# Optimization experiments

Measured on AMD Instinct MI355X. Metric: run time of the kernel, lower is better.

Reference implementation:

```python
import jax, jax.numpy as jnp
import numpy as np

HEADS, DIM_HEAD, LANDMARKS, PINV_ITERS, RES_K = 8, 64, 256, 6, 33
DIM = 512


def layer_norm(x, w, b, eps=1e-5):
    mu = x.mean(-1, keepdims=True)
    var = ((x - mu) ** 2).mean(-1, keepdims=True)
    return (x - mu) * jax.lax.rsqrt(var + eps) * w + b


def moore_penrose_pinv(x, iters=PINV_ITERS):
    # x: (b, h, m, m)
    abs_x = jnp.abs(x)
    col = abs_x.sum(-1)
    row = abs_x.sum(-2)
    z = jnp.swapaxes(x, -1, -2) / (jnp.max(col) * jnp.max(row))
    I = jnp.eye(x.shape[-1], dtype=x.dtype)
    for _ in range(iters):
        xz = x @ z
        z = 0.25 * z @ (13.0 * I - xz @ (15.0 * I - xz @ (7.0 * I - xz)))
    return z


def nystrom_attention(x, qkv_w, out_w, out_b, res_kernel):
    b, n, _ = x.shape
    h, dh, m = HEADS, DIM_HEAD, LANDMARKS
    l = n // m  # seq chosen divisible by landmarks
    qkv = x @ qkv_w  # (b, n, 3*h*dh)
    q, k, v = jnp.split(qkv, 3, axis=-1)
    def to_heads(t):
        return t.reshape(b, n, h, dh).transpose(0, 2, 1, 3)  # (b,h,n,dh)
    q, k, v = to_heads(q), to_heads(k), to_heads(v)
    q = q * (dh ** -0.5)
    # landmark pooling: mean over contiguous groups of size l
    q_l = q.reshape(b, h, m, l, dh).mean(axis=3)  # (b,h,m,dh)
    k_l = k.reshape(b, h, m, l, dh).mean(axis=3)
    attn1 = jax.nn.softmax(jnp.einsum('bhid,bhjd->bhij', q, k_l), axis=-1)   # (b,h,n,m)
    attn2 = jax.nn.softmax(jnp.einsum('bhid,bhjd->bhij', q_l, k_l), axis=-1) # (b,h,m,m)
    attn3 = jax.nn.softmax(jnp.einsum('bhid,bhjd->bhij', q_l, k), axis=-1)   # (b,h,m,n)
    attn2_inv = moore_penrose_pinv(attn2)
    out = (attn1 @ attn2_inv) @ (attn3 @ v)  # (b,h,n,dh)
    # depthwise residual conv over sequence dim, per head
    pad = (RES_K - 1) // 2
    out = out + jax.lax.conv_general_dilated(
        v, res_kernel, window_strides=(1, 1), padding=((pad, pad), (0, 0)),
        dimension_numbers=('NCHW', 'OIHW', 'NCHW'), feature_group_count=h)
    out = out.transpose(0, 2, 1, 3).reshape(b, n, h * dh)
    return out @ out_w + out_b


def trans_layer(x, p):
    return x + nystrom_attention(layer_norm(x, p['norm_w'], p['norm_b']),
                                 p['qkv_w'], p['out_w'], p['out_b'], p['res_k'])


def setup_inputs() -> dict:
    key = jax.random.key(0)
    ks = jax.random.split(key, 20)
    N, F = 16383, 1024
    d = {}
    d['x'] = jax.random.normal(ks[0], (1, N, F), dtype=jnp.float32)
    d['fc_w'] = jax.random.normal(ks[1], (F, DIM), dtype=jnp.float32) * 0.03
    d['fc_b'] = jnp.zeros((DIM,), dtype=jnp.float32)
    d['cls_token'] = jax.random.normal(ks[2], (1, 1, DIM), dtype=jnp.float32) * 1e-6
    for i, base in [(3, 'l1'), (9, 'l2')]:
        d[base + '_norm_w'] = jnp.ones((DIM,), dtype=jnp.float32)
        d[base + '_norm_b'] = jnp.zeros((DIM,), dtype=jnp.float32)
        d[base + '_qkv_w'] = jax.random.normal(ks[i], (DIM, 3 * DIM), dtype=jnp.float32) * 0.03
        d[base + '_out_w'] = jax.random.normal(ks[i + 1], (DIM, DIM), dtype=jnp.float32) * 0.03
        d[base + '_out_b'] = jnp.zeros((DIM,), dtype=jnp.float32)
        d[base + '_res_k'] = jax.random.normal(ks[i + 2], (HEADS, 1, RES_K, 1), dtype=jnp.float32) * 0.1
    d['norm_w'] = jnp.ones((DIM,), dtype=jnp.float32)
    d['norm_b'] = jnp.zeros((DIM,), dtype=jnp.float32)
    d['clf_w'] = jax.random.normal(ks[15], (DIM, 4), dtype=jnp.float32) * 0.05
    d['clf_b'] = jnp.zeros((4,), dtype=jnp.float32)
    return d


def reference(x, fc_w, fc_b, cls_token, l1_norm_w, l1_norm_b, l1_qkv_w, l1_out_w,
              l1_out_b, l1_res_k, l2_norm_w, l2_norm_b, l2_qkv_w, l2_out_w,
              l2_out_b, l2_res_k, norm_w, norm_b, clf_w, clf_b):
    h = jax.nn.relu(x @ fc_w + fc_b)                       # (1, N, 512)
    h = jnp.concatenate([cls_token, h], axis=1)            # (1, N+1, 512)
    p1 = dict(norm_w=l1_norm_w, norm_b=l1_norm_b, qkv_w=l1_qkv_w,
              out_w=l1_out_w, out_b=l1_out_b, res_k=l1_res_k)
    p2 = dict(norm_w=l2_norm_w, norm_b=l2_norm_b, qkv_w=l2_qkv_w,
              out_w=l2_out_w, out_b=l2_out_b, res_k=l2_res_k)
    h = trans_layer(h, p1)
    h = trans_layer(h, p2)
    h = layer_norm(h, norm_w, norm_b)[:, 0]                # (1, 512)
    logits = h @ clf_w + clf_b                             # (1, n_classes)
    hazards = jax.nn.sigmoid(logits)
    S = jnp.cumprod(1.0 - hazards, axis=1)
    return (hazards, S)
```

## Files before the change

### kernel.cpp

```cpp
#include <hip/hip_runtime.h>

#define NTOK 16384
#define NDIM 512
#define STP_LD 280

typedef __attribute__((ext_vector_type(8))) short short8;
typedef __attribute__((ext_vector_type(4))) float f32x4;

__device__ __forceinline__ unsigned short f2bf(float f) {
  unsigned u = __float_as_uint(f);
  u += 0x7fffu + ((u >> 16) & 1u);
  return (unsigned short)(u >> 16);
}
__device__ __forceinline__ float bf2f(unsigned short u) {
  return __uint_as_float((unsigned)u << 16);
}

__device__ __forceinline__ void gload_lds16(const void* g, void* l) {
  __builtin_amdgcn_global_load_lds(
      (const __attribute__((address_space(1))) unsigned int*)(unsigned long long)(g),
      (__attribute__((address_space(3))) unsigned int*)(unsigned long long)(l), 16, 0, 0);
}

template<int EPI>
__global__ __launch_bounds__(256) void gemm_bf16(
    const unsigned short* __restrict__ A, const unsigned short* __restrict__ Bt,
    float* __restrict__ C, const float* __restrict__ bias,
    int M, int N, int K, int Mstore)
{
  __shared__ unsigned short As[2][128 * 32];
  __shared__ unsigned short Bs[2][128 * 32];
  const int tid = threadIdx.x;
  const int row0 = blockIdx.y * 128, col0 = blockIdx.x * 128;
  const int wave = tid >> 6, lane = tid & 63;
  const int wm = (wave >> 1) * 64, wn = (wave & 1) * 64;
  const int quad = lane >> 4, m16 = lane & 15;

  const int r0 = tid >> 2;
  const int c8 = (tid & 3) * 8;
  const unsigned short* Ag0 = A + (size_t)(row0 + r0) * K + c8;
  const unsigned short* Ag1 = A + (size_t)(row0 + r0 + 64) * K + c8;
  const unsigned short* Bg0 = Bt + (size_t)(col0 + r0) * K + c8;
  const unsigned short* Bg1 = Bt + (size_t)(col0 + r0 + 64) * K + c8;
  char* AsB = (char*)As;
  char* BsB = (char*)Bs;
  const int wb = wave * 1024;

  f32x4 acc[4][4] = {};
  const int nc = K >> 5;
  gload_lds16(Ag0, AsB + wb);
  gload_lds16(Ag1, AsB + 4096 + wb);
  gload_lds16(Bg0, BsB + wb);
  gload_lds16(Bg1, BsB + 4096 + wb);
  __syncthreads();
  int b = 0;
  for (int c = 0; c < nc; c++) {
    if (c + 1 < nc) {
      int k1 = (c + 1) * 32;
      gload_lds16(Ag0 + k1, AsB + (b ^ 1) * 8192 + wb);
      gload_lds16(Ag1 + k1, AsB + (b ^ 1) * 8192 + 4096 + wb);
      gload_lds16(Bg0 + k1, BsB + (b ^ 1) * 8192 + wb);
      gload_lds16(Bg1 + k1, BsB + (b ^ 1) * 8192 + 4096 + wb);
    }
    short8 af[4], bf[4];
#pragma unroll
    for (int i = 0; i < 4; i++) {
      af[i] = *(const short8*)&As[b][(wm + i * 16 + m16) * 32 + quad * 8];
      bf[i] = *(const short8*)&Bs[b][(wn + i * 16 + m16) * 32 + quad * 8];
    }
#pragma unroll
    for (int i = 0; i < 4; i++)
#pragma unroll
      for (int j = 0; j < 4; j++)
        acc[i][j] = __builtin_amdgcn_mfma_f32_16x16x32_bf16(af[i], bf[j], acc[i][j], 0, 0, 0);
    __syncthreads();
    b ^= 1;
  }
#pragma unroll
  for (int i = 0; i < 4; i++) {
#pragma unroll
    for (int r = 0; r < 4; r++) {
      int gr = row0 + wm + i * 16 + quad * 4 + r;
      if (gr < Mstore) {
#pragma unroll
        for (int j = 0; j < 4; j++) {
          int gc = col0 + wn + j * 16 + m16;
          float v = acc[i][j][r];
          if (EPI == 1) { v += bias[gc]; v = fmaxf(v, 0.f); }
          if (EPI == 2) { v += bias[gc] + C[(size_t)gr * N + gc]; }
          C[(size_t)gr * N + gc] = v;
        }
      }
    }
  }
}

template<bool WN, bool WT, bool WF>
__global__ __launch_bounds__(256) void bmm_pinv64(
    const unsigned short* __restrict__ A, const unsigned short* __restrict__ Bt,
    unsigned short* __restrict__ Cn, unsigned short* __restrict__ Ct,
    float* __restrict__ Cf,
    float an, float bn, float at, float bt)
{
  const int hh = blockIdx.z;
  A  += (size_t)hh << 16;
  Bt += (size_t)hh << 16;
  __shared__ unsigned short As[2][64 * 32];
  __shared__ unsigned short Bs[2][64 * 32];
  const int tid = threadIdx.x;
  const int row0 = blockIdx.y * 64, col0 = blockIdx.x * 64;
  const int wave = tid >> 6, lane = tid & 63;
  const int wm = (wave >> 1) * 32, wn = (wave & 1) * 32;
  const int quad = lane >> 4, m16 = lane & 15;
  const int sr = wave * 16 + (lane >> 2);
  const int sc = (lane & 3) * 8;
  const unsigned short* Ag = A + (size_t)(row0 + sr) * 256 + sc;
  const unsigned short* Bg = Bt + (size_t)(col0 + sr) * 256 + sc;
  char* AsW = (char*)As + wave * 1024;
  char* BsW = (char*)Bs + wave * 1024;

  f32x4 acc[2][2] = {};
  gload_lds16(Ag, AsW);
  gload_lds16(Bg, BsW);
  __syncthreads();
  int b = 0;
  for (int c = 0; c < 8; c++) {
    if (c < 7) {
      gload_lds16(Ag + (c + 1) * 32, AsW + (b ^ 1) * 4096);
      gload_lds16(Bg + (c + 1) * 32, BsW + (b ^ 1) * 4096);
    }
    short8 af[2], bfr[2];
#pragma unroll
    for (int i = 0; i < 2; i++) {
      af[i]  = *(const short8*)&As[b][(wm + i * 16 + m16) * 32 + quad * 8];
      bfr[i] = *(const short8*)&Bs[b][(wn + i * 16 + m16) * 32 + quad * 8];
    }
#pragma unroll
    for (int i = 0; i < 2; i++)
#pragma unroll
      for (int j = 0; j < 2; j++)
        acc[i][j] = __builtin_amdgcn_mfma_f32_16x16x32_bf16(af[i], bfr[j], acc[i][j], 0, 0, 0);
    __syncthreads();
    b ^= 1;
  }
  unsigned short* CnH = Cn + ((size_t)hh << 16);
  unsigned short* CtH = Ct + ((size_t)hh << 16);
  float* CfH = WF ? (Cf + ((size_t)hh << 16)) : nullptr;
#pragma unroll
  for (int i = 0; i < 2; i++) {
#pragma unroll
    for (int r = 0; r < 4; r++) {
      int gr = row0 + wm + i * 16 + quad * 4 + r;
#pragma unroll
      for (int j = 0; j < 2; j++) {
        int gc = col0 + wn + j * 16 + m16;
        float p = acc[i][j][r];
        float diag = (gr == gc) ? 1.f : 0.f;
        if (WN) {
          unsigned short nb_ = f2bf(an * p + bn * diag);
          CnH[(size_t)gr * 256 + gc] = nb_;
          if (WF) CfH[(size_t)gr * 256 + gc] = bf2f(nb_);
        }
        if (WT) CtH[(size_t)gc * 256 + gr] = f2bf(at * p + bt * diag);
      }
    }
  }
}

__global__ void castpad_x(const float* __restrict__ x, unsigned short* __restrict__ xb,
                          size_t nvalid) {
  size_t i4 = ((size_t)blockIdx.x * 256 + threadIdx.x) * 4;
  float4 v = make_float4(0.f, 0.f, 0.f, 0.f);
  if (i4 < nvalid) v = *(const float4*)(x + i4);
  ushort4 o;
  o.x = f2bf(v.x); o.y = f2bf(v.y); o.z = f2bf(v.z); o.w = f2bf(v.w);
  *(ushort4*)(xb + i4) = o;
}

__global__ __launch_bounds__(256) void transpose_cast(
    const float* __restrict__ in, unsigned short* __restrict__ out, int R, int C)
{
  __shared__ float tile[32][33];
  int r0 = blockIdx.x * 32, c0 = blockIdx.y * 32;
  int tx = threadIdx.x & 31, ty = threadIdx.x >> 5;
  for (int yy = ty; yy < 32; yy += 8)
    tile[yy][tx] = in[(size_t)(r0 + yy) * C + c0 + tx];
  __syncthreads();
  for (int yy = ty; yy < 32; yy += 8)
    out[(size_t)(c0 + yy) * R + r0 + tx] = f2bf(tile[tx][yy]);
}

__global__ __launch_bounds__(1024) void qkv_prep(
    const float* __restrict__ qkv,
    unsigned short* __restrict__ qb, unsigned short* __restrict__ kb,
    float* __restrict__ q_l, float* __restrict__ k_lT,
    unsigned short* __restrict__ q_lb, unsigned short* __restrict__ k_lb)
{
  const int j = blockIdx.x, t = threadIdx.x;
  const int cs = t & 255, rg = t >> 8;
  const int c = cs * 4;
  const bool isq = c < 512;
  __shared__ float4 pbuf[4][256];
  float4 acc = make_float4(0.f, 0.f, 0.f, 0.f);
  for (int r = rg * 16; r < rg * 16 + 16; r++) {
    int row = j * 64 + r;
    float4 v = *(const float4*)(qkv + (size_t)row * 1536 + c);
    acc.x += v.x; acc.y += v.y; acc.z += v.z; acc.w += v.w;
    ushort4 o;
    if (isq) {
      o.x = f2bf(v.x * 0.125f); o.y = f2bf(v.y * 0.125f);
      o.z = f2bf(v.z * 0.125f); o.w = f2bf(v.w * 0.125f);
      *(ushort4*)(qb + (size_t)row * 512 + c) = o;
    } else {
      o.x = f2bf(v.x); o.y = f2bf(v.y); o.z = f2bf(v.z); o.w = f2bf(v.w);
      *(ushort4*)(kb + (size_t)row * 512 + (c - 512)) = o;
    }
  }
  pbuf[rg][cs] = acc;
  __syncthreads();
  if (rg == 0) {
    float4 a0 = pbuf[0][cs], a1 = pbuf[1][cs], a2 = pbuf[2][cs], a3 = pbuf[3][cs];
    float sc = (1.f / 64.f) * (isq ? 0.125f : 1.f);
    float4 p;
    p.x = (a0.x + a1.x + a2.x + a3.x) * sc;
    p.y = (a0.y + a1.y + a2.y + a3.y) * sc;
    p.z = (a0.z + a1.z + a2.z + a3.z) * sc;
    p.w = (a0.w + a1.w + a2.w + a3.w) * sc;
    int cc = isq ? c : c - 512;
    int hh = cc >> 6, d = cc & 63;
    size_t o = ((size_t)(hh * 256 + j)) * 64 + d;
    ushort4 ob;
    ob.x = f2bf(p.x); ob.y = f2bf(p.y); ob.z = f2bf(p.z); ob.w = f2bf(p.w);
    if (isq) {
      *(float4*)(q_l + o) = p; *(ushort4*)(q_lb + o) = ob;
    } else {
      size_t of = ((size_t)hh << 14) + (j >> 6) * 4096 + (d >> 5) * 2048
                + ((j >> 4) & 3) * 512 + ((d >> 3) & 3) * 128 + (j & 15) * 8 + (d & 7);
      *(ushort4*)(k_lb + of) = ob;
      float* kt = k_lT + ((size_t)hh * 64 + d) * 256 + j;
      kt[0] = p.x; kt[256] = p.y; kt[512] = p.z; kt[768] = p.w;
    }
  }
}

__global__ __launch_bounds__(256) void transpose_cast_v(
    const float* __restrict__ qkv, unsigned short* __restrict__ vTb)
{
  __shared__ float tile[32][33];
  int i0 = blockIdx.x * 32, c0 = blockIdx.y * 32;
  int tx = threadIdx.x & 31, ty = threadIdx.x >> 5;
  for (int yy = ty; yy < 32; yy += 8)
    tile[yy][tx] = qkv[(size_t)(i0 + yy) * 1536 + 1024 + c0 + tx];
  __syncthreads();
  for (int yy = ty; yy < 32; yy += 8)
    vTb[(size_t)(c0 + yy) * NTOK + i0 + tx] = f2bf(tile[tx][yy]);
}

__global__ __launch_bounds__(256) void conv_seq(
    const unsigned short* __restrict__ vTb, const float* __restrict__ res_k,
    unsigned short* __restrict__ convT)
{
  const int c = blockIdx.y;
  const int h = c >> 6;
  const int i0 = (blockIdx.x * 256 + threadIdx.x) * 8;
  float rk[33];
#pragma unroll
  for (int u = 0; u < 33; u++) rk[u] = res_k[h * 33 + u];
  const unsigned short* vr = vTb + (size_t)c * NTOK;
  float win[40];
#pragma unroll
  for (int ch = 0; ch < 5; ch++) {
    int a = i0 - 16 + ch * 8;
    if (a >= 0 && a < NTOK) {
      ushort4 u0 = *(const ushort4*)(vr + a);
      ushort4 u1 = *(const ushort4*)(vr + a + 4);
      win[ch * 8 + 0] = bf2f(u0.x); win[ch * 8 + 1] = bf2f(u0.y);
      win[ch * 8 + 2] = bf2f(u0.z); win[ch * 8 + 3] = bf2f(u0.w);
      win[ch * 8 + 4] = bf2f(u1.x); win[ch * 8 + 5] = bf2f(u1.y);
      win[ch * 8 + 6] = bf2f(u1.z); win[ch * 8 + 7] = bf2f(u1.w);
    } else {
#pragma unroll
      for (int u = 0; u < 8; u++) win[ch * 8 + u] = 0.f;
    }
  }
  ushort4 o0, o1;
  float out[8];
#pragma unroll
  for (int jj = 0; jj < 8; jj++) {
    float s = 0.f;
#pragma unroll
    for (int u = 0; u < 33; u++) s += rk[u] * win[jj + u];
    out[jj] = s;
  }
  o0.x = f2bf(out[0]); o0.y = f2bf(out[1]); o0.z = f2bf(out[2]); o0.w = f2bf(out[3]);
  o1.x = f2bf(out[4]); o1.y = f2bf(out[5]); o1.z = f2bf(out[6]); o1.w = f2bf(out[7]);
  *(ushort4*)(convT + (size_t)c * NTOK + i0) = o0;
  *(ushort4*)(convT + (size_t)c * NTOK + i0 + 4) = o1;
}

template<bool W2>
__global__ __launch_bounds__(256) void bmm_f32(
    const float* __restrict__ A, const float* __restrict__ B, float* __restrict__ C,
    float* __restrict__ C2, int M, int N, int K, float alpha, float beta, float gamma)
{
  const int h = blockIdx.z;
  A += (size_t)h * M * K; B += (size_t)h * K * N;
  size_t cb = (size_t)h * M * N;
  __shared__ float As[16][64];
  __shared__ float Bs[16][64];
  const int tid = threadIdx.x;
  const int row0 = blockIdx.y * 64, col0 = blockIdx.x * 64;
  const int ty = tid >> 4, tx = tid & 15;
  const int ar = tid >> 2, ac = (tid & 3) << 2;
  const int bk = tid >> 4, bj = (tid & 15) << 2;
  float acc[4][4] = {};
  float4 a  = *(const float4*)(A + (size_t)(row0 + ar) * K + ac);
  float4 bv = *(const float4*)(B + (size_t)bk * N + col0 + bj);
  for (int k0 = 0; k0 < K; k0 += 16) {
    As[ac + 0][ar] = a.x; As[ac + 1][ar] = a.y; As[ac + 2][ar] = a.z; As[ac + 3][ar] = a.w;
    *(float4*)&Bs[bk][bj] = bv;
    __syncthreads();
    if (k0 + 16 < K) {
      a  = *(const float4*)(A + (size_t)(row0 + ar) * K + k0 + 16 + ac);
      bv = *(const float4*)(B + (size_t)(k0 + 16 + bk) * N + col0 + bj);
    }
#pragma unroll
    for (int kk = 0; kk < 16; kk++) {
      float4 av = *(float4*)&As[kk][ty << 2];
      float4 bvv = *(float4*)&Bs[kk][tx << 2];
      float a4[4] = {av.x, av.y, av.z, av.w};
      float b4[4] = {bvv.x, bvv.y, bvv.z, bvv.w};
#pragma unroll
      for (int ii = 0; ii < 4; ii++)
#pragma unroll
        for (int jj = 0; jj < 4; jj++) acc[ii][jj] += a4[ii] * b4[jj];
    }
    __syncthreads();
  }
#pragma unroll
  for (int ii = 0; ii < 4; ii++) {
    int gr = row0 + (ty << 2) + ii;
#pragma unroll
    for (int jj = 0; jj < 4; jj++) {
      int gc = col0 + (tx << 2) + jj;
      float diag = (gr == gc) ? 1.f : 0.f;
      float v = alpha * acc[ii][jj] + beta * diag;
      C[cb + (size_t)gr * N + gc] = v;
      if (W2) C2[cb + (size_t)gr * N + gc] = gamma * diag - v;
    }
  }
}

__global__ void cls_copy(const float* __restrict__ cls, float* __restrict__ h) {
  int t = threadIdx.x;
  if (t < 512) h[t] = cls[t];
}

__global__ __launch_bounds__(256) void layernorm_rows(
    const float* __restrict__ x, unsigned short* __restrict__ y,
    const float* __restrict__ w, const float* __restrict__ b)
{
  const int row = blockIdx.x, tid = threadIdx.x;
  const float* xr = x + (size_t)row * NDIM;
  float2 v = ((const float2*)xr)[tid];
  float sum = v.x + v.y, sq = v.x * v.x + v.y * v.y;
#pragma unroll
  for (int off = 32; off; off >>= 1) { sum += __shfl_xor(sum, off); sq += __shfl_xor(sq, off); }
  __shared__ float r1[4], r2[4];
  if ((tid & 63) == 0) { r1[tid >> 6] = sum; r2[tid >> 6] = sq; }
  __syncthreads();
  sum = r1[0] + r1[1] + r1[2] + r1[3];
  sq  = r2[0] + r2[1] + r2[2] + r2[3];
  float mu = sum * (1.f / 512.f);
  float var = sq * (1.f / 512.f) - mu * mu;
  float rs = rsqrtf(var + 1e-5f);
  float a = (v.x - mu) * rs * w[2 * tid]     + b[2 * tid];
  float c = (v.y - mu) * rs * w[2 * tid + 1] + b[2 * tid + 1];
  ((unsigned*)(y + (size_t)row * NDIM))[tid] = (unsigned)f2bf(a) | ((unsigned)f2bf(c) << 16);
}

__global__ __launch_bounds__(256) void attn2_softmax(
    const float* __restrict__ q_l, const float* __restrict__ k_lT,
    float* __restrict__ x2, unsigned short* __restrict__ x2b)
{
  int row = blockIdx.x, h = blockIdx.y, j = threadIdx.x;
  __shared__ float qrow[64];
  __shared__ float red[4];
  if (j < 64) qrow[j] = q_l[(size_t)(h * 256 + row) * 64 + j];
  __syncthreads();
  const float* kt = k_lT + ((size_t)h * 64) * 256 + j;
  float s = 0.f;
#pragma unroll 8
  for (int d = 0; d < 64; d++) s += qrow[d] * kt[(size_t)d * 256];
  float m = s;
#pragma unroll
  for (int off = 32; off; off >>= 1) m = fmaxf(m, __shfl_xor(m, off));
  if ((j & 63) == 0) red[j >> 6] = m;
  __syncthreads();
  m = fmaxf(fmaxf(red[0], red[1]), fmaxf(red[2], red[3]));
  __syncthreads();
  float e = __expf(s - m), l = e;
#pragma unroll
  for (int off = 32; off; off >>= 1) l += __shfl_xor(l, off);
  if ((j & 63) == 0) red[j >> 6] = l;
  __syncthreads();
  l = red[0] + red[1] + red[2] + red[3];
  float val = e / l;
  size_t o = ((size_t)(h * 256 + row) << 8) + j;
  x2[o] = val;
  x2b[o] = f2bf(val);
}

__global__ __launch_bounds__(256) void colrow_max(const float* __restrict__ x2,
                                                  float* __restrict__ scal)
{
  const int h = blockIdx.x, tid = threadIdx.x;
  const float* xh = x2 + ((size_t)h << 16);
  float mx = -1e30f;
  if (blockIdx.y == 0) {
    const int wave = tid >> 6, lane = tid & 63;
    for (int r = wave; r < 256; r += 4) {
      float4 v = *(const float4*)(xh + (size_t)r * 256 + lane * 4);
      float s = v.x + v.y + v.z + v.w;
#pragma unroll
      for (int off = 32; off; off >>= 1) s += __shfl_xor(s, off);
      mx = fmaxf(mx, s);
    }
  } else {
    float cs = 0.f;
    for (int r0 = 0; r0 < 256; r0 += 8) {
      float v[8];
#pragma unroll
      for (int u = 0; u < 8; u++) v[u] = xh[(size_t)(r0 + u) * 256 + tid];
#pragma unroll
      for (int u = 0; u < 8; u++) cs += v[u];
    }
    mx = cs;
  }
#pragma unroll
  for (int off = 32; off; off >>= 1) mx = fmaxf(mx, __shfl_xor(mx, off));
  __shared__ float red[4];
  if ((tid & 63) == 0) red[tid >> 6] = mx;
  __syncthreads();
  if (tid == 0) {
    float m = fmaxf(fmaxf(red[0], red[1]), fmaxf(red[2], red[3]));
    atomicMax((unsigned int*)&scal[blockIdx.y], __float_as_uint(m));
  }
}

__global__ void zinit_bf(const float* __restrict__ x2, unsigned short* __restrict__ zb,
                         unsigned short* __restrict__ zTb, const float* __restrict__ scal)
{
  int idx = blockIdx.x * 256 + threadIdx.x;
  int hh = idx >> 16, i = (idx >> 8) & 255, j = idx & 255;
  float den = scal[0] * scal[1];
  float val = x2[idx] / den;
  unsigned short b = f2bf(val);
  zTb[idx] = b;
  zb[(hh << 16) + (j << 8) + i] = b;
}

__global__ __launch_bounds__(256) void flash_fused(
    const unsigned short* __restrict__ q_lb, const unsigned short* __restrict__ kb,
    const unsigned short* __restrict__ vTb,
    float* __restrict__ Opart, float* __restrict__ mlpart)
{
  const int ks = blockIdx.x, qg = blockIdx.y, h = blockIdx.z;
  const int tid = threadIdx.x;
  const int wave = tid >> 6, lane = tid & 63;
  const int quad = lane >> 4, m16 = lane & 15;

  __shared__ unsigned short Ks[2][4096];
  __shared__ unsigned short Vs[2][4096];
  __shared__ unsigned short pbuf_all[4][16 * 72];
  unsigned short* pbuf = pbuf_all[wave];

  const int key00 = ks * 512;

  const int sr  = (wave << 3) + (lane >> 3);
  const int sxz = (lane & 7) ^ ((lane >> 3) & 7);
  const unsigned short* kst0 = kb + (size_t)(key00 + sr) * 512 + (h << 6) + sxz * 8;
  const unsigned short* kst1 = kst0 + (size_t)32 * 512;
  const unsigned short* vst0 = vTb + (size_t)((h << 6) + sr) * NTOK + key00 + sxz * 8;
  const unsigned short* vst1 = vst0 + (size_t)32 * NTOK;
  char* ldsKw = (char*)&Ks[0][0] + (wave << 10);
  char* ldsVw = (char*)&Vs[0][0] + (wave << 10);

  const int xs  = m16 & 7;
  const int co0 = ((quad) ^ xs) << 3;
  const int co1 = ((4 + quad) ^ xs) << 3;

  const int qrow_w = qg * 64 + wave * 16;
  const unsigned short* qbase = q_lb + ((size_t)h << 14) + (size_t)(qrow_w + m16) * 64;
  short8 aq0 = *(const short8*)(qbase + quad * 8);
  short8 aq1 = *(const short8*)(qbase + 32 + quad * 8);

  float m_e[4], l_e[4];
#pragma unroll
  for (int e = 0; e < 4; e++) { m_e[e] = -1e30f; l_e[e] = 0.f; }
  f32x4 acc_o[4] = {};

#define FF_STAGE(bb, cc) do {                                   \
    size_t ko = (size_t)(cc) * 32768; int vo = (cc) * 64;       \
    gload_lds16(kst0 + ko, ldsKw + (bb) * 8192);                \
    gload_lds16(kst1 + ko, ldsKw + (bb) * 8192 + 4096);         \
    gload_lds16(vst0 + vo, ldsVw + (bb) * 8192);                \
    gload_lds16(vst1 + vo, ldsVw + (bb) * 8192 + 4096);         \
  } while (0)

  FF_STAGE(0, 0);
  __syncthreads();
  int b = 0;
  for (int c = 0; c < 8; c++) {
    if (c < 7) FF_STAGE(b ^ 1, c + 1);
    const unsigned short* Kb = Ks[b];
    const unsigned short* Vb = Vs[b];
    f32x4 s[4] = {};
    __builtin_amdgcn_s_setprio(1);
#pragma unroll
    for (int kt = 0; kt < 4; kt++) {
      const unsigned short* krow = Kb + ((kt << 4) + m16) * 64;
      short8 b0 = *(const short8*)(krow + co0);
      short8 b1 = *(const short8*)(krow + co1);
      s[kt] = __builtin_amdgcn_mfma_f32_16x16x32_bf16(aq0, b0, s[kt], 0, 0, 0);
      s[kt] = __builtin_amdgcn_mfma_f32_16x16x32_bf16(aq1, b1, s[kt], 0, 0, 0);
    }
    __builtin_amdgcn_s_setprio(0);
#pragma unroll
    for (int e = 0; e < 4; e++) {
      float mx = fmaxf(fmaxf(s[0][e], s[1][e]), fmaxf(s[2][e], s[3][e]));
      mx = fmaxf(mx, __shfl_xor(mx, 1));
      mx = fmaxf(mx, __shfl_xor(mx, 2));
      mx = fmaxf(mx, __shfl_xor(mx, 4));
      mx = fmaxf(mx, __shfl_xor(mx, 8));
      float mn = fmaxf(m_e[e], mx);
      float scale = __expf(m_e[e] - mn);
      m_e[e] = mn;
      float sum = 0.f;
#pragma unroll
      for (int kt = 0; kt < 4; kt++) {
        float ev = __expf(s[kt][e] - mn);
        s[kt][e] = ev;
        sum += ev;
      }
      sum += __shfl_xor(sum, 1); sum += __shfl_xor(sum, 2);
      sum += __shfl_xor(sum, 4); sum += __shfl_xor(sum, 8);
      l_e[e] = l_e[e] * scale + sum;
#pragma unroll
      for (int dt = 0; dt < 4; dt++) acc_o[dt][e] *= scale;
    }
#pragma unroll
    for (int kt = 0; kt < 4; kt++)
#pragma unroll
      for (int e = 0; e < 4; e++)
        pbuf[(quad * 4 + e) * 72 + kt * 16 + m16] = f2bf(s[kt][e]);
    asm volatile("s_waitcnt lgkmcnt(0)" ::: "memory");
    short8 ap0 = *(const short8*)&pbuf[m16 * 72 + quad * 8];
    short8 ap1 = *(const short8*)&pbuf[m16 * 72 + 32 + quad * 8];
    __builtin_amdgcn_s_setprio(1);
#pragma unroll
    for (int dt = 0; dt < 4; dt++) {
      const unsigned short* vrow = Vb + ((dt << 4) + m16) * 64;
      short8 bv0 = *(const short8*)(vrow + co0);
      short8 bv1 = *(const short8*)(vrow + co1);
      acc_o[dt] = __builtin_amdgcn_mfma_f32_16x16x32_bf16(ap0, bv0, acc_o[dt], 0, 0, 0);
      acc_o[dt] = __builtin_amdgcn_mfma_f32_16x16x32_bf16(ap1, bv1, acc_o[dt], 0, 0, 0);
    }
    __builtin_amdgcn_s_setprio(0);
    __syncthreads();
    b ^= 1;
  }
#undef FF_STAGE
  float* ob = Opart + ((size_t)(ks * 8 + h) * 256 + qrow_w) * 64;
#pragma unroll
  for (int dt = 0; dt < 4; dt++)
#pragma unroll
    for (int e = 0; e < 4; e++)
      ob[(size_t)(quad * 4 + e) * 64 + dt * 16 + m16] = acc_o[dt][e];
  if (m16 == 0) {
    float* mlb = mlpart + ((size_t)(ks * 8 + h) * 256 + qrow_w) * 2;
#pragma unroll
    for (int e = 0; e < 4; e++) {
      mlb[(quad * 4 + e) * 2]     = m_e[e];
      mlb[(quad * 4 + e) * 2 + 1] = l_e[e];
    }
  }
}

__global__ __launch_bounds__(256) void flash_merge(
    const float* __restrict__ Opart, const float* __restrict__ mlpart,
    float* __restrict__ kv)
{
  const int rc = blockIdx.x, h = blockIdx.y, tid = threadIdx.x;
  const int r = rc * 32 + (tid >> 3);
  const int d0 = (tid & 7) * 8;
  float M = -1e30f;
  for (int ks = 0; ks < 32; ks++)
    M = fmaxf(M, mlpart[((size_t)(ks * 8 + h) * 256 + r) * 2]);
  float L = 0.f;
  float o[8];
#pragma unroll
  for (int j = 0; j < 8; j++) o[j] = 0.f;
  for (int ks = 0; ks < 32; ks++) {
    const float* mlb = mlpart + ((size_t)(ks * 8 + h) * 256 + r) * 2;
    float w = __expf(mlb[0] - M);
    L += mlb[1] * w;
    const float* op = Opart + ((size_t)(ks * 8 + h) * 256 + r) * 64 + d0;
    float4 a = *(const float4*)op;
    float4 b = *(const float4*)(op + 4);
    o[0] += a.x * w; o[1] += a.y * w; o[2] += a.z * w; o[3] += a.w * w;
    o[4] += b.x * w; o[5] += b.y * w; o[6] += b.z * w; o[7] += b.w * w;
  }
  float invL = 1.f / L;
  float* out = kv + ((size_t)(h * 256 + r)) * 64 + d0;
#pragma unroll
  for (int j = 0; j < 8; j++) out[j] = o[j] * invL;
}

__global__ __launch_bounds__(256) void bmt_kernel(
    const float* __restrict__ zf, const float* __restrict__ kv,
    unsigned short* __restrict__ BmT)
{
  const int jb = blockIdx.x, hh = blockIdx.y, tid = threadIdx.x;
  __shared__ float zt[64 * 256];
  const float* zsrc = zf + ((size_t)hh << 16) + (size_t)(jb * 64) * 256;
  for (int rep = 0; rep < 16; rep++) {
    int e4 = (rep * 256 + tid) * 4;
    *(float4*)&zt[e4] = *(const float4*)(zsrc + e4);
  }
  __syncthreads();
  const int d = tid & 63, jg = tid >> 6;
  const float* kvh = kv + ((size_t)hh << 14) + d;
  float acc[16];
#pragma unroll
  for (int u = 0; u < 16; u++) acc[u] = 0.f;
  for (int k0 = 0; k0 < 256; k0 += 8) {
    float kv8[8];
#pragma unroll
    for (int u = 0; u < 8; u++) kv8[u] = kvh[(size_t)(k0 + u) << 6];
#pragma unroll
    for (int jj = 0; jj < 16; jj++) {
      const float* zr = &zt[(jg * 16 + jj) * 256 + k0];
#pragma unroll
      for (int u = 0; u < 8; u++) acc[jj] += zr[u] * kv8[u];
    }
  }
  unsigned short* obh = BmT + ((size_t)hh << 14) + (d >> 5) * 8192
                        + ((d >> 4) & 1) * 512 + (d & 15) * 8;
#pragma unroll
  for (int jj = 0; jj < 16; jj++) {
    int j = jb * 64 + jg * 16 + jj;
    obh[(j >> 5) * 1024 + ((j >> 3) & 3) * 128 + (j & 7)] = f2bf(acc[jj]);
  }
}

__global__ __launch_bounds__(256) void attn1_out(
    const unsigned short* __restrict__ qb, const unsigned short* __restrict__ k_lb,
    const unsigned short* __restrict__ BmT, const unsigned short* __restrict__ convT,
    unsigned short* __restrict__ attn_out)
{
  const int qc = blockIdx.x, h = blockIdx.y, tid = threadIdx.x;
  const int q0 = qc * 32;
  const int wave = tid >> 6, lane = tid & 63;
  const int quad = lane >> 4, m16 = lane & 15;

  __shared__ unsigned short stp[32 * STP_LD];
  __shared__ float redm[4][32], redl[4][32];

  const int mi3 = (wave & 1) * 16;
  const int nbase = (wave >> 1) * 32;
  const int gi0 = q0 + mi3 + quad * 4;
  ushort4 cv4_[2];
#pragma unroll
  for (int t = 0; t < 2; t++) {
    int d = nbase + t * 16 + m16;
    cv4_[t] = *(const ushort4*)(convT + (size_t)((h << 6) + d) * NTOK + gi0);
  }

  f32x4 acc1[2][4] = {};
  {
    const unsigned short* qbase = qb + (size_t)q0 * 512 + (h << 6);
    const unsigned short* kf = k_lb + ((size_t)h << 14) + (wave << 12);
#pragma unroll
    for (int kc = 0; kc < 2; kc++) {
      short8 aq[2], bk[4];
#pragma unroll
      for (int i = 0; i < 2; i++)
        aq[i] = *(const short8*)(qbase + (size_t)(i * 16 + m16) * 512 + kc * 32 + quad * 8);
#pragma unroll
      for (int n = 0; n < 4; n++)
        bk[n] = *(const short8*)(kf + kc * 2048 + n * 512 + lane * 8);
#pragma unroll
      for (int i = 0; i < 2; i++)
#pragma unroll
        for (int n = 0; n < 4; n++)
          acc1[i][n] = __builtin_amdgcn_mfma_f32_16x16x32_bf16(aq[i], bk[n], acc1[i][n], 0, 0, 0);
    }
  }
#pragma unroll
  for (int i = 0; i < 2; i++) {
#pragma unroll
    for (int e = 0; e < 4; e++) {
      float mx = fmaxf(fmaxf(acc1[i][0][e], acc1[i][1][e]), fmaxf(acc1[i][2][e], acc1[i][3][e]));
      mx = fmaxf(mx, __shfl_xor(mx, 1));
      mx = fmaxf(mx, __shfl_xor(mx, 2));
      mx = fmaxf(mx, __shfl_xor(mx, 4));
      mx = fmaxf(mx, __shfl_xor(mx, 8));
      if (m16 == 0) redm[wave][i * 16 + quad * 4 + e] = mx;
    }
  }
  __syncthreads();
#pragma unroll
  for (int i = 0; i < 2; i++) {
#pragma unroll
    for (int e = 0; e < 4; e++) {
      int r = i * 16 + quad * 4 + e;
      float gm = fmaxf(fmaxf(redm[0][r], redm[1][r]), fmaxf(redm[2][r], redm[3][r]));
      float s = 0.f;
#pragma unroll
      for (int n = 0; n < 4; n++) {
        float ev = __expf(acc1[i][n][e] - gm);
        acc1[i][n][e] = ev;
        s += ev;
      }
      s += __shfl_xor(s, 1); s += __shfl_xor(s, 2);
      s += __shfl_xor(s, 4); s += __shfl_xor(s, 8);
      if (m16 == 0) redl[wave][r] = s;
    }
  }
#pragma unroll
  for (int i = 0; i < 2; i++)
#pragma unroll
    for (int n = 0; n < 4; n++) {
      int col = wave * 64 + n * 16 + m16;
#pragma unroll
      for (int e = 0; e < 4; e++)
        stp[(i * 16 + quad * 4 + e) * STP_LD + col] = f2bf(acc1[i][n][e]);
    }
  __syncthreads();

  f32x4 acc3[2] = {};
  {
    const unsigned short* bf_ = BmT + ((size_t)h << 14) + ((nbase >> 5) << 13);
#pragma unroll
    for (int kc = 0; kc < 8; kc++) {
      short8 ap = *(const short8*)&stp[(mi3 + m16) * STP_LD + kc * 32 + quad * 8];
#pragma unroll
      for (int t = 0; t < 2; t++) {
        short8 bp = *(const short8*)(bf_ + kc * 1024 + t * 512 + lane * 8);
        acc3[t] = __builtin_amdgcn_mfma_f32_16x16x32_bf16(ap, bp, acc3[t], 0, 0, 0);
      }
    }
  }
#pragma unroll
  for (int t = 0; t < 2; t++) {
    int d = nbase + t * 16 + m16;
    unsigned short cvs[4] = {cv4_[t].x, cv4_[t].y, cv4_[t].z, cv4_[t].w};
#pragma unroll
    for (int e = 0; e < 4; e++) {
      int lr = mi3 + quad * 4 + e;
      float l = redl[0][lr] + redl[1][lr] + redl[2][lr] + redl[3][lr];
      float v = acc3[t][e] / l + bf2f(cvs[e]);
      attn_out[((size_t)(gi0 + e) << 9) + (h << 6) + d] = f2bf(v);
    }
  }
}

__global__ __launch_bounds__(256) void final_head(
    const float* __restrict__ hrow, const float* __restrict__ nw, const float* __restrict__ nb,
    const float* __restrict__ cw, const float* __restrict__ cb, float* __restrict__ out)
{
  const int tid = threadIdx.x;
  __shared__ float ln0[512];
  __shared__ float r1[4], r2[4];
  __shared__ float lg[4][4];
  float2 v = ((const float2*)hrow)[tid];
  float sum = v.x + v.y, sq = v.x * v.x + v.y * v.y;
#pragma unroll
  for (int off = 32; off; off >>= 1) { sum += __shfl_xor(sum, off); sq += __shfl_xor(sq, off); }
  if ((tid & 63) == 0) { r1[tid >> 6] = sum; r2[tid >> 6] = sq; }
  __syncthreads();
  sum = r1[0] + r1[1] + r1[2] + r1[3];
  sq  = r2[0] + r2[1] + r2[2] + r2[3];
  float mu = sum * (1.f / 512.f);
  float var = sq * (1.f / 512.f) - mu * mu;
  float rs = rsqrtf(var + 1e-5f);
  ln0[2 * tid]     = (v.x - mu) * rs * nw[2 * tid]     + nb[2 * tid];
  ln0[2 * tid + 1] = (v.y - mu) * rs * nw[2 * tid + 1] + nb[2 * tid + 1];
  __syncthreads();
  float p[4] = {0.f, 0.f, 0.f, 0.f};
  for (int k = tid; k < 512; k += 256) {
    float lv = ln0[k];
#pragma unroll
    for (int c = 0; c < 4; c++) p[c] += lv * cw[k * 4 + c];
  }
#pragma unroll
  for (int off = 32; off; off >>= 1)
#pragma unroll
    for (int c = 0; c < 4; c++) p[c] += __shfl_xor(p[c], off);
  if ((tid & 63) == 0) {
    int w = tid >> 6;
#pragma unroll
    for (int c = 0; c < 4; c++) lg[w][c] = p[c];
  }
  __syncthreads();
  if (tid == 0) {
    float cum = 1.f;
    for (int c = 0; c < 4; c++) {
      float logit = lg[0][c] + lg[1][c] + lg[2][c] + lg[3][c] + cb[c];
      float hz = 1.f / (1.f + __expf(-logit));
      out[c] = hz;
      cum *= (1.f - hz);
      out[4 + c] = cum;
    }
  }
}

extern "C" void kernel_launch(void* const* d_in, const int* in_sizes, int n_in,
                              void* d_out, int out_size, void* d_ws, size_t ws_size,
                              hipStream_t stream)
{
  (void)in_sizes; (void)n_in; (void)out_size; (void)ws_size;
  const float* x    = (const float*)d_in[0];
  const float* fc_w = (const float*)d_in[1];
  const float* fc_b = (const float*)d_in[2];
  const float* cls  = (const float*)d_in[3];
  const float* nw[2]   = {(const float*)d_in[4],  (const float*)d_in[10]};
  const float* nb[2]   = {(const float*)d_in[5],  (const float*)d_in[11]};
  const float* qkvw[2] = {(const float*)d_in[6],  (const float*)d_in[12]};
  const float* outw[2] = {(const float*)d_in[7],  (const float*)d_in[13]};
  const float* outb[2] = {(const float*)d_in[8],  (const float*)d_in[14]};
  const float* resk[2] = {(const float*)d_in[9],  (const float*)d_in[15]};
  const float* fnw = (const float*)d_in[16];
  const float* fnb = (const float*)d_in[17];
  const float* cw  = (const float*)d_in[18];
  const float* cb  = (const float*)d_in[19];

  float* ws = (float*)d_ws;
  float* h    = ws; ws += (size_t)NTOK * NDIM;
  float* qkv  = ws; ws += (size_t)NTOK * 1536;
  float* bigv = ws; ws += (size_t)(512 * NTOK) / 2;
  float* q_l  = ws; ws += 8 * 256 * 64;
  float* k_lT = ws; ws += 8 * 256 * 64;
  float* x2   = ws; ws += 8 * 256 * 256;
  float* zf   = ws; ws += 8 * 256 * 256;
  float* zfin = ws; ws += 8 * 256 * 256;
  float* tA   = ws; ws += 8 * 256 * 256;
  float* tB   = ws; ws += 8 * 256 * 256;
  float* tC   = ws; ws += 8 * 256 * 256;
  float* kv   = ws; ws += 8 * 256 * 64;
  float* scal = ws; ws += 64;
  unsigned short* actb = (unsigned short*)ws; ws += (size_t)NTOK * NDIM / 2;
  unsigned short* wT   = (unsigned short*)ws; ws += (1536 * 512) / 2;
  unsigned short* qb   = (unsigned short*)ws; ws += (size_t)NTOK * NDIM / 2;
  unsigned short* k_lb = (unsigned short*)ws; ws += (8 * 256 * 64) / 2;
  unsigned short* q_lb = (unsigned short*)ws; ws += (8 * 256 * 64) / 2;
  unsigned short* x2b  = (unsigned short*)ws; ws += (8 * 256 * 256) / 2;
  unsigned short* zb0  = (unsigned short*)ws; ws += (8 * 256 * 256) / 2;
  unsigned short* zb1  = (unsigned short*)ws; ws += (8 * 256 * 256) / 2;
  unsigned short* zT0  = (unsigned short*)ws; ws += (8 * 256 * 256) / 2;
  unsigned short* zT1  = (unsigned short*)ws; ws += (8 * 256 * 256) / 2;
  unsigned short* xzb  = (unsigned short*)ws; ws += (8 * 256 * 256) / 2;
  unsigned short* t1T  = (unsigned short*)ws; ws += (8 * 256 * 256) / 2;
  unsigned short* t2T  = (unsigned short*)ws; ws += (8 * 256 * 256) / 2;
  unsigned short* t3T  = (unsigned short*)ws; ws += (8 * 256 * 256) / 2;
  unsigned short* BmT  = (unsigned short*)ws; ws += (8 * 64 * 256) / 2;

  unsigned short* xb  = (unsigned short*)qkv;
  unsigned short* kb  = actb;
  unsigned short* vTb = (unsigned short*)bigv;
  float* Opart  = qkv;
  float* mlpart = qkv + (size_t)32 * 8 * 256 * 64;
  unsigned short* convT = (unsigned short*)(qkv + (size_t)32 * 8 * 256 * 64 + 32 * 8 * 256 * 2);

  unsigned short* zbp[2] = {zb0, zb1};
  unsigned short* zTp[2] = {zT0, zT1};

  castpad_x<<<16384, 256, 0, stream>>>(x, xb, (size_t)16383 * 1024);
  transpose_cast<<<dim3(32, 16), 256, 0, stream>>>(fc_w, wT, 1024, 512);
  gemm_bf16<1><<<dim3(4, 128), 256, 0, stream>>>(xb, wT, h + 512, fc_b,
                                                 16384, 512, 1024, 16383);
  cls_copy<<<1, 512, 0, stream>>>(cls, h);

  for (int L = 0; L < 2; L++) {
    layernorm_rows<<<NTOK, 256, 0, stream>>>(h, actb, nw[L], nb[L]);
    transpose_cast<<<dim3(16, 48), 256, 0, stream>>>(qkvw[L], wT, 512, 1536);
    gemm_bf16<0><<<dim3(12, 128), 256, 0, stream>>>(actb, wT, qkv, nullptr,
                                                    NTOK, 1536, 512, NTOK);
    qkv_prep<<<256, 1024, 0, stream>>>(qkv, qb, kb, q_l, k_lT, q_lb, k_lb);
    transpose_cast_v<<<dim3(512, 16), 256, 0, stream>>>(qkv, vTb);
    attn2_softmax<<<dim3(256, 8), 256, 0, stream>>>(q_l, k_lT, x2, x2b);
    hipMemsetAsync(scal, 0, 2 * sizeof(float), stream);
    colrow_max<<<dim3(8, 2), 256, 0, stream>>>(x2, scal);
    zinit_bf<<<2048, 256, 0, stream>>>(x2, zbp[0], zTp[0], scal);

    flash_fused<<<dim3(32, 4, 8), 256, 0, stream>>>(q_lb, kb, vTb, Opart, mlpart);
    flash_merge<<<dim3(8, 8), 256, 0, stream>>>(Opart, mlpart, kv);
    conv_seq<<<dim3(8, 512), 256, 0, stream>>>(vTb, resk[L], convT);

    int cur = 0;
    dim3 pg(4, 4, 8);
    for (int it = 0; it < 5; it++) {
      bmm_pinv64<true,  true, false><<<pg, 256, 0, stream>>>(x2b, zTp[cur], xzb, t1T, nullptr,
                                                             1.f, 0.f, -1.f, 7.f);
      bmm_pinv64<false, true, false><<<pg, 256, 0, stream>>>(xzb, t1T, nullptr, t2T, nullptr,
                                                             0.f, 0.f, -1.f, 15.f);
      bmm_pinv64<false, true, false><<<pg, 256, 0, stream>>>(xzb, t2T, nullptr, t3T, nullptr,
                                                             0.f, 0.f, -1.f, 13.f);
      if (it < 4)
        bmm_pinv64<true, true, false><<<pg, 256, 0, stream>>>(zbp[cur], t3T, zbp[cur ^ 1],
                                                              zTp[cur ^ 1], nullptr,
                                                              0.25f, 0.f, 0.25f, 0.f);
      else
        bmm_pinv64<true, true, true><<<pg, 256, 0, stream>>>(zbp[cur], t3T, zbp[cur ^ 1],
                                                             zTp[cur ^ 1], zf,
                                                             0.25f, 0.f, 0.25f, 0.f);
      cur ^= 1;
    }
    bmm_f32<true ><<<dim3(4, 4, 8), 256, 0, stream>>>(x2, zf, tA, tB, 256, 256, 256, 1.f, 0.f, 7.f);
    bmm_f32<false><<<dim3(4, 4, 8), 256, 0, stream>>>(tA, tB, tC, nullptr, 256, 256, 256, -1.f, 15.f, 0.f);
    bmm_f32<false><<<dim3(4, 4, 8), 256, 0, stream>>>(tA, tC, tB, nullptr, 256, 256, 256, -1.f, 13.f, 0.f);
    bmm_f32<false><<<dim3(4, 4, 8), 256, 0, stream>>>(zf, tB, zfin, nullptr, 256, 256, 256, 0.25f, 0.f, 0.f);

    bmt_kernel<<<dim3(4, 8), 256, 0, stream>>>(zfin, kv, BmT);
    attn1_out<<<dim3(512, 8), 256, 0, stream>>>(qb, k_lb, BmT, convT, actb);
    transpose_cast<<<dim3(16, 16), 256, 0, stream>>>(outw[L], wT, 512, 512);
    gemm_bf16<2><<<dim3(4, 128), 256, 0, stream>>>(actb, wT, h, outb[L],
                                                   NTOK, 512, 512, NTOK);
  }
  final_head<<<1, 256, 0, stream>>>(h, fnw, fnb, cw, cb, (float*)d_out);
}
```

Measured before the change: 1.019 ms.

## Fuse QKV GEMM epilogue with bf16 casts, landmark pooling and V transpose

New measurement: 951.1 us. 6.6% less time.

```diff
diff --git a/kernel.cpp b/kernel.cpp
--- a/kernel.cpp
+++ b/kernel.cpp
@@ -31,7 +31,11 @@
   __shared__ unsigned short As[2][128 * 32];
   __shared__ unsigned short Bs[2][128 * 32];
   const int tid = threadIdx.x;
-  const int row0 = blockIdx.y * 128, col0 = blockIdx.x * 128;
+  const int id = blockIdx.y * gridDim.x + blockIdx.x;
+  const int nwg8 = (gridDim.x * gridDim.y) >> 3;
+  const int logical = (id & 7) * nwg8 + (id >> 3);
+  const int row0 = (logical / gridDim.x) * 128;
+  const int col0 = (logical % gridDim.x) * 128;
   const int wave = tid >> 6, lane = tid & 63;
   const int wm = (wave >> 1) * 64, wn = (wave & 1) * 64;
   const int quad = lane >> 4, m16 = lane & 15;
@@ -89,6 +93,138 @@
           if (EPI == 1) { v += bias[gc]; v = fmaxf(v, 0.f); }
           if (EPI == 2) { v += bias[gc] + C[(size_t)gr * N + gc]; }
           C[(size_t)gr * N + gc] = v;
+        }
+      }
+    }
+  }
+}
+
+__global__ __launch_bounds__(256) void qkv_gemm(
+    const unsigned short* __restrict__ A, const unsigned short* __restrict__ Bt,
+    unsigned short* __restrict__ qb, unsigned short* __restrict__ kb,
+    unsigned short* __restrict__ vTb,
+    float* __restrict__ q_l, float* __restrict__ k_lT,
+    unsigned short* __restrict__ q_lb, unsigned short* __restrict__ k_lb)
+{
+  __shared__ unsigned short As[2][128 * 32];
+  __shared__ unsigned short Bs[2][128 * 32];
+  __shared__ unsigned short vt[128 * 136];
+  const int tid = threadIdx.x;
+  const int id = blockIdx.y * gridDim.x + blockIdx.x;
+  const int nwg8 = (gridDim.x * gridDim.y) >> 3;
+  const int logical = (id & 7) * nwg8 + (id >> 3);
+  const int bx = logical % 12, by = logical / 12;
+  const int row0 = by * 128, col0 = bx * 128;
+  const int wave = tid >> 6, lane = tid & 63;
+  const int wm = (wave >> 1) * 64, wn = (wave & 1) * 64;
+  const int quad = lane >> 4, m16 = lane & 15;
+
+  const int r0 = tid >> 2;
+  const int c8 = (tid & 3) * 8;
+  const unsigned short* Ag0 = A + (size_t)(row0 + r0) * 512 + c8;
+  const unsigned short* Ag1 = A + (size_t)(row0 + r0 + 64) * 512 + c8;
+  const unsigned short* Bg0 = Bt + (size_t)(col0 + r0) * 512 + c8;
+  const unsigned short* Bg1 = Bt + (size_t)(col0 + r0 + 64) * 512 + c8;
+  char* AsB = (char*)As;
+  char* BsB = (char*)Bs;
+  const int wb = wave * 1024;
+
+  f32x4 acc[4][4] = {};
+  gload_lds16(Ag0, AsB + wb);
+  gload_lds16(Ag1, AsB + 4096 + wb);
+  gload_lds16(Bg0, BsB + wb);
+  gload_lds16(Bg1, BsB + 4096 + wb);
+  __syncthreads();
+  int b = 0;
+  for (int c = 0; c < 16; c++) {
+    if (c < 15) {
+      int k1 = (c + 1) * 32;
+      gload_lds16(Ag0 + k1, AsB + (b ^ 1) * 8192 + wb);
+      gload_lds16(Ag1 + k1, AsB + (b ^ 1) * 8192 + 4096 + wb);
+      gload_lds16(Bg0 + k1, BsB + (b ^ 1) * 8192 + wb);
+      gload_lds16(Bg1 + k1, BsB + (b ^ 1) * 8192 + 4096 + wb);
+    }
+    short8 af[4], bf[4];
+#pragma unroll
+    for (int i = 0; i < 4; i++) {
+      af[i] = *(const short8*)&As[b][(wm + i * 16 + m16) * 32 + quad * 8];
+      bf[i] = *(const short8*)&Bs[b][(wn + i * 16 + m16) * 32 + quad * 8];
+    }
+#pragma unroll
+    for (int i = 0; i < 4; i++)
+#pragma unroll
+      for (int j = 0; j < 4; j++)
+        acc[i][j] = __builtin_amdgcn_mfma_f32_16x16x32_bf16(af[i], bf[j], acc[i][j], 0, 0, 0);
+    __syncthreads();
+    b ^= 1;
+  }
+
+  const int sel = bx >> 2;
+  if (sel == 2) {
+#pragma unroll
+    for (int i = 0; i < 4; i++)
+#pragma unroll
+      for (int j = 0; j < 4; j++) {
+        int c_l = wn + j * 16 + m16;
+        int r_b = wm + i * 16 + quad * 4;
+        ushort4 o;
+        o.x = f2bf(acc[i][j][0]); o.y = f2bf(acc[i][j][1]);
+        o.z = f2bf(acc[i][j][2]); o.w = f2bf(acc[i][j][3]);
+        *(ushort4*)&vt[c_l * 136 + r_b] = o;
+      }
+    __syncthreads();
+    const int gc0 = col0 - 1024;
+    const int u = tid & 15, cc = tid >> 4;
+#pragma unroll
+    for (int pass = 0; pass < 8; pass++) {
+      int c = pass * 16 + cc;
+      short8 v8 = *(const short8*)&vt[c * 136 + u * 8];
+      *(short8*)(vTb + (size_t)(gc0 + c) * NTOK + row0 + u * 8) = v8;
+    }
+  } else {
+    const bool isq = (sel == 0);
+#pragma unroll
+    for (int i = 0; i < 4; i++)
+#pragma unroll
+      for (int r = 0; r < 4; r++) {
+        int gr = row0 + wm + i * 16 + quad * 4 + r;
+#pragma unroll
+        for (int j = 0; j < 4; j++) {
+          int gc = col0 + wn + j * 16 + m16;
+          float v = acc[i][j][r];
+          if (isq) qb[(size_t)gr * 512 + gc] = f2bf(v * 0.125f);
+          else     kb[(size_t)gr * 512 + (gc - 512)] = f2bf(v);
+        }
+      }
+    float ps[4];
+#pragma unroll
+    for (int j = 0; j < 4; j++) {
+      float s = 0.f;
+#pragma unroll
+      for (int i = 0; i < 4; i++)
+#pragma unroll
+        for (int r = 0; r < 4; r++) s += acc[i][j][r];
+      s += __shfl_xor(s, 16);
+      s += __shfl_xor(s, 32);
+      ps[j] = s;
+    }
+    if (quad == 0) {
+      const int jg = by * 2 + (wm >> 6);
+      const float sc = isq ? (0.125f / 64.f) : (1.f / 64.f);
+#pragma unroll
+      for (int j = 0; j < 4; j++) {
+        int gc = col0 + wn + j * 16 + m16 - (isq ? 0 : 512);
+        int hh = gc >> 6, d = gc & 63;
+        float p = ps[j] * sc;
+        if (isq) {
+          size_t o = ((size_t)(hh * 256 + jg)) * 64 + d;
+          q_l[o] = p;
+          q_lb[o] = f2bf(p);
+        } else {
+          k_lT[((size_t)hh * 64 + d) * 256 + jg] = p;
+          size_t of = ((size_t)hh << 14) + (jg >> 6) * 4096 + (d >> 5) * 2048
+                    + ((jg >> 4) & 3) * 512 + ((d >> 3) & 3) * 128 + (jg & 15) * 8 + (d & 7);
+          k_lb[of] = f2bf(p);
         }
       }
     }
@@ -188,72 +324,6 @@
   __syncthreads();
   for (int yy = ty; yy < 32; yy += 8)
     out[(size_t)(c0 + yy) * R + r0 + tx] = f2bf(tile[tx][yy]);
-}
-
-__global__ __launch_bounds__(1024) void qkv_prep(
-    const float* __restrict__ qkv,
-    unsigned short* __restrict__ qb, unsigned short* __restrict__ kb,
-    float* __restrict__ q_l, float* __restrict__ k_lT,
-    unsigned short* __restrict__ q_lb, unsigned short* __restrict__ k_lb)
-{
-  const int j = blockIdx.x, t = threadIdx.x;
-  const int cs = t & 255, rg = t >> 8;
-  const int c = cs * 4;
-  const bool isq = c < 512;
-  __shared__ float4 pbuf[4][256];
-  float4 acc = make_float4(0.f, 0.f, 0.f, 0.f);
-  for (int r = rg * 16; r < rg * 16 + 16; r++) {
-    int row = j * 64 + r;
-    float4 v = *(const float4*)(qkv + (size_t)row * 1536 + c);
-    acc.x += v.x; acc.y += v.y; acc.z += v.z; acc.w += v.w;
-    ushort4 o;
-    if (isq) {
-      o.x = f2bf(v.x * 0.125f); o.y = f2bf(v.y * 0.125f);
-      o.z = f2bf(v.z * 0.125f); o.w = f2bf(v.w * 0.125f);
-      *(ushort4*)(qb + (size_t)row * 512 + c) = o;
-    } else {
-      o.x = f2bf(v.x); o.y = f2bf(v.y); o.z = f2bf(v.z); o.w = f2bf(v.w);
-      *(ushort4*)(kb + (size_t)row * 512 + (c - 512)) = o;
-    }
-  }
-  pbuf[rg][cs] = acc;
-  __syncthreads();
-  if (rg == 0) {
-    float4 a0 = pbuf[0][cs], a1 = pbuf[1][cs], a2 = pbuf[2][cs], a3 = pbuf[3][cs];
-    float sc = (1.f / 64.f) * (isq ? 0.125f : 1.f);
-    float4 p;
-    p.x = (a0.x + a1.x + a2.x + a3.x) * sc;
-    p.y = (a0.y + a1.y + a2.y + a3.y) * sc;
-    p.z = (a0.z + a1.z + a2.z + a3.z) * sc;
-    p.w = (a0.w + a1.w + a2.w + a3.w) * sc;
-    int cc = isq ? c : c - 512;
-    int hh = cc >> 6, d = cc & 63;
-    size_t o = ((size_t)(hh * 256 + j)) * 64 + d;
-    ushort4 ob;
-    ob.x = f2bf(p.x); ob.y = f2bf(p.y); ob.z = f2bf(p.z); ob.w = f2bf(p.w);
-    if (isq) {
-      *(float4*)(q_l + o) = p; *(ushort4*)(q_lb + o) = ob;
-    } else {
-      size_t of = ((size_t)hh << 14) + (j >> 6) * 4096 + (d >> 5) * 2048
-                + ((j >> 4) & 3) * 512 + ((d >> 3) & 3) * 128 + (j & 15) * 8 + (d & 7);
-      *(ushort4*)(k_lb + of) = ob;
-      float* kt = k_lT + ((size_t)hh * 64 + d) * 256 + j;
-      kt[0] = p.x; kt[256] = p.y; kt[512] = p.z; kt[768] = p.w;
-    }
-  }
-}
-
-__global__ __launch_bounds__(256) void transpose_cast_v(
-    const float* __restrict__ qkv, unsigned short* __restrict__ vTb)
-{
-  __shared__ float tile[32][33];
-  int i0 = blockIdx.x * 32, c0 = blockIdx.y * 32;
-  int tx = threadIdx.x & 31, ty = threadIdx.x >> 5;
-  for (int yy = ty; yy < 32; yy += 8)
-    tile[yy][tx] = qkv[(size_t)(i0 + yy) * 1536 + 1024 + c0 + tx];
-  __syncthreads();
-  for (int yy = ty; yy < 32; yy += 8)
-    vTb[(size_t)(c0 + yy) * NTOK + i0 + tx] = f2bf(tile[tx][yy]);
 }
 
 __global__ __launch_bounds__(256) void conv_seq(
@@ -865,9 +935,9 @@
   unsigned short* t2T  = (unsigned short*)ws; ws += (8 * 256 * 256) / 2;
   unsigned short* t3T  = (unsigned short*)ws; ws += (8 * 256 * 256) / 2;
   unsigned short* BmT  = (unsigned short*)ws; ws += (8 * 64 * 256) / 2;
+  unsigned short* kbuf = (unsigned short*)ws; ws += (size_t)NTOK * NDIM / 2;
 
   unsigned short* xb  = (unsigned short*)qkv;
-  unsigned short* kb  = actb;
   unsigned short* vTb = (unsigned short*)bigv;
   float* Opart  = qkv;
   float* mlpart = qkv + (size_t)32 * 8 * 256 * 64;
@@ -885,16 +955,14 @@
   for (int L = 0; L < 2; L++) {
     layernorm_rows<<<NTOK, 256, 0, stream>>>(h, actb, nw[L], nb[L]);
     transpose_cast<<<dim3(16, 48), 256, 0, stream>>>(qkvw[L], wT, 512, 1536);
-    gemm_bf16<0><<<dim3(12, 128), 256, 0, stream>>>(actb, wT, qkv, nullptr,
-                                                    NTOK, 1536, 512, NTOK);
-    qkv_prep<<<256, 1024, 0, stream>>>(qkv, qb, kb, q_l, k_lT, q_lb, k_lb);
-    transpose_cast_v<<<dim3(512, 16), 256, 0, stream>>>(qkv, vTb);
+    qkv_gemm<<<dim3(12, 128), 256, 0, stream>>>(actb, wT, qb, kbuf, vTb,
+                                                q_l, k_lT, q_lb, k_lb);
     attn2_softmax<<<dim3(256, 8), 256, 0, stream>>>(q_l, k_lT, x2, x2b);
     hipMemsetAsync(scal, 0, 2 * sizeof(float), stream);
     colrow_max<<<dim3(8, 2), 256, 0, stream>>>(x2, scal);
     zinit_bf<<<2048, 256, 0, stream>>>(x2, zbp[0], zTp[0], scal);
 
-    flash_fused<<<dim3(32, 4, 8), 256, 0, stream>>>(q_lb, kb, vTb, Opart, mlpart);
+    flash_fused<<<dim3(32, 4, 8), 256, 0, stream>>>(q_lb, kbuf, vTb, Opart, mlpart);
     flash_merge<<<dim3(8, 8), 256, 0, stream>>>(Opart, mlpart, kv);
     conv_seq<<<dim3(8, 512), 256, 0, stream>>>(vTb, resk[L], convT);
 
```
